# Optimization experiments

Hardware: AMD Instinct MI355X
Metric: run time of the kernel (lower is better)

The kernel has to match this reference:

```python
import jax, jax.numpy as jnp
import numpy as np

B, IMG, P, CIN = 4, 384, 16, 3
G = IMG // P            # 24 patches per side
NP = G * G              # 576 patch tokens
N = NP + 1              # +cls
D, H, L, MLP, NC = 768, 12, 12, 3072, 1000
HD = D // H
SCALE = HD ** -0.5
NUM_REL = (2 * G - 1) * (2 * G - 1) + 3   # (2*1-1)*(2G-1)*(2G-1)+3 = 2212
EPS = 1e-6


def gen_rel_index():
    # window (1, G, G): depth diff is always 0, reduces to 2D BEiT indexing
    coords = np.stack(np.meshgrid(np.arange(G), np.arange(G), indexing='ij')).reshape(2, -1)
    rel = (coords[:, :, None] - coords[:, None, :]).transpose(1, 2, 0).copy()  # (NP,NP,2)
    rel[:, :, 0] += G - 1
    rel[:, :, 1] += G - 1
    rel[:, :, 0] *= 2 * G - 1
    idx = np.zeros((N, N), dtype=np.int32)
    idx[1:, 1:] = rel.sum(-1)
    idx[0, :] = NUM_REL - 3
    idx[:, 0] = NUM_REL - 2
    idx[0, 0] = NUM_REL - 1
    return jnp.asarray(idx)


def setup_inputs() -> dict:
    key = jax.random.key(0)
    ks = jax.random.split(key, 20)
    s = 0.02
    inp = {
        'x': jax.random.normal(ks[0], (B, CIN, IMG, IMG), jnp.float32),
        'patch_w': s * jax.random.normal(ks[1], (D, CIN * P * P), jnp.float32),
        'patch_b': jnp.zeros((D,), jnp.float32),
        'cls_token': s * jax.random.normal(ks[2], (1, 1, D), jnp.float32),
        'pos_embed': s * jax.random.normal(ks[3], (1, N, D), jnp.float32),
        'ln1_w': jnp.ones((L, D), jnp.float32),
        'ln1_b': jnp.zeros((L, D), jnp.float32),
        'qkv_w': s * jax.random.normal(ks[4], (L, 3 * D, D), jnp.float32),
        'q_bias': jnp.zeros((L, D), jnp.float32),
        'v_bias': jnp.zeros((L, D), jnp.float32),
        'proj_w': s * jax.random.normal(ks[5], (L, D, D), jnp.float32),
        'proj_b': jnp.zeros((L, D), jnp.float32),
        'ln2_w': jnp.ones((L, D), jnp.float32),
        'ln2_b': jnp.zeros((L, D), jnp.float32),
        'fc1_w': s * jax.random.normal(ks[6], (L, MLP, D), jnp.float32),
        'fc1_b': jnp.zeros((L, MLP), jnp.float32),
        'fc2_w': s * jax.random.normal(ks[7], (L, D, MLP), jnp.float32),
        'fc2_b': jnp.zeros((L, D), jnp.float32),
        'rel_table': s * jax.random.normal(ks[8], (L, NUM_REL, H), jnp.float32),
        'fc_norm_w': jnp.ones((D,), jnp.float32),
        'fc_norm_b': jnp.zeros((D,), jnp.float32),
        'head_w': s * jax.random.normal(ks[9], (NC, D), jnp.float32),
        'head_b': jnp.zeros((NC,), jnp.float32),
        'rel_index': gen_rel_index(),
    }
    return inp


def _ln(x, w, b):
    m = x.mean(-1, keepdims=True)
    v = ((x - m) ** 2).mean(-1, keepdims=True)
    return (x - m) * jax.lax.rsqrt(v + EPS) * w + b


def _beit_fwd(x, patch_w, patch_b, cls_token, pos_embed,
              ln1_w, ln1_b, qkv_w, q_bias, v_bias, proj_w, proj_b,
              ln2_w, ln2_b, fc1_w, fc1_b, fc2_w, fc2_b, rel_table,
              fc_norm_w, fc_norm_b, head_w, head_b, rel_index):
    # patch embed: conv P x P stride P == reshape + matmul; patch vec order (c, ph, pw)
    patches = x.reshape(B, CIN, G, P, G, P).transpose(0, 2, 4, 1, 3, 5).reshape(B, NP, CIN * P * P)
    tok = patches @ patch_w.T + patch_b                      # (B, NP, D)
    h = jnp.concatenate([jnp.broadcast_to(cls_token, (B, 1, D)), tok], axis=1) + pos_embed

    def block(h, p):
        l1w, l1b, qw, qb, vb, pw, pb, l2w, l2b, f1w, f1b, f2w, f2b, rt = p
        y = _ln(h, l1w, l1b)
        bias = jnp.concatenate([qb, jnp.zeros_like(qb), vb])  # k_bias frozen zeros
        qkv = (y @ qw.T + bias).reshape(B, N, 3, H, HD).transpose(2, 0, 3, 1, 4)
        q, k, v = qkv[0] * SCALE, qkv[1], qkv[2]              # (B,H,N,HD)
        attn = jnp.einsum('bhnd,bhmd->bhnm', q, k)
        rel = rt[rel_index].transpose(2, 0, 1)                # (H,N,N)
        attn = jax.nn.softmax(attn + rel[None], axis=-1)
        o = jnp.einsum('bhnm,bhmd->bhnd', attn, v).transpose(0, 2, 1, 3).reshape(B, N, D)
        h = h + (o @ pw.T + pb)
        y = _ln(h, l2w, l2b)
        y = jax.nn.gelu(y @ f1w.T + f1b, approximate=False) @ f2w.T + f2b
        return h + y, None

    xs = (ln1_w, ln1_b, qkv_w, q_bias, v_bias, proj_w, proj_b,
          ln2_w, ln2_b, fc1_w, fc1_b, fc2_w, fc2_b, rel_table)
    h, _ = jax.lax.scan(block, h, xs)

    pooled = h[:, 1:].mean(axis=1)                            # global_pool='avg' drops cls
    return _ln(pooled, fc_norm_w, fc_norm_b) @ head_w.T + head_b  # (B, NC)


def reference(x, patch_w, patch_b, cls_token, pos_embed,
              ln1_w, ln1_b, qkv_w, q_bias, v_bias, proj_w, proj_b,
              ln2_w, ln2_b, fc1_w, fc1_b, fc2_w, fc2_b, rel_table,
              fc_norm_w, fc_norm_b, head_w, head_b, rel_index):
    return _beit_fwd(x, patch_w, patch_b, cls_token, pos_embed,
                     ln1_w, ln1_b, qkv_w, q_bias, v_bias, proj_w, proj_b,
                     ln2_w, ln2_b, fc1_w, fc1_b, fc2_w, fc2_b, rel_table,
                     fc_norm_w, fc_norm_b, head_w, head_b, rel_index)
```

## Files before the change

### kernel.cpp

```cpp
#include <hip/hip_runtime.h>
#include <math.h>

typedef unsigned short u16;
typedef __bf16 bf16x8_t __attribute__((ext_vector_type(8)));
typedef u16 u16x8 __attribute__((ext_vector_type(8)));
typedef float f32x4 __attribute__((ext_vector_type(4)));

#define CBATCH 4
#define CN 577
#define CNP 576
#define CD 768
#define CH 12
#define CHD 64
#define CL 12
#define CMLP 3072
#define CVP 640
#define CROWS (CBATCH*CN)
#define CROWSP 2432
#define CNN2 332929
#define CBH (CBATCH*CH)
#define CSKP 2
#define CSKF 4
#define CMT 37

__device__ __forceinline__ float b2f(u16 u){
  unsigned x = ((unsigned)u) << 16;
  return __builtin_bit_cast(float, x);
}
__device__ __forceinline__ u16 f2b(float f){
  unsigned x = __builtin_bit_cast(unsigned, f);
  unsigned r = x + 0x7fffu + ((x >> 16) & 1u);
  return (u16)(r >> 16);
}

__device__ __forceinline__ f32x4 MFMA(u16x8 a, u16x8 b, f32x4 c){
  return __builtin_amdgcn_mfma_f32_16x16x32_bf16(
      __builtin_bit_cast(bf16x8_t, a), __builtin_bit_cast(bf16x8_t, b), c, 0, 0, 0);
}

__device__ __forceinline__ void gl_lds16(const u16* g, u16* l){
  __builtin_amdgcn_global_load_lds(
      (const __attribute__((address_space(1))) unsigned int*)g,
      (__attribute__((address_space(3))) unsigned int*)l, 16, 0, 0);
}

__device__ __forceinline__ int xcd_chunk(int o, int nwg){
  int q8 = nwg >> 3, r8 = nwg & 7;
  int xcd = o & 7, sl = o >> 3;
  return (xcd < r8 ? xcd*(q8+1) : r8*(q8+1) + (xcd - r8)*q8) + sl;
}


__global__ void cvt_kernel(const float* __restrict__ src, u16* __restrict__ dst, int n){
  int i = (blockIdx.x * 256 + threadIdx.x) * 4;
  if(i < n){
    float4 v = *reinterpret_cast<const float4*>(src + i);
    ushort4 o;
    o.x = f2b(v.x); o.y = f2b(v.y); o.z = f2b(v.z); o.w = f2b(v.w);
    *reinterpret_cast<ushort4*>(dst + i) = o;
  }
}

__global__ void zero_kernel(u16* __restrict__ p, int n){
  int i = (blockIdx.x * 256 + threadIdx.x) * 8;
  if(i < n){
    u16x8 z = {0,0,0,0,0,0,0,0};
    *reinterpret_cast<u16x8*>(p + i) = z;
  }
}

__global__ void im2col_kernel(const float* __restrict__ x, u16* __restrict__ out){
  int id = blockIdx.x * 256 + threadIdx.x;
  if(id >= 2304*768) return;
  int col = id % 768, row = id / 768;
  int b = row / 576, p = row % 576;
  int gy = p / 24, gx = p % 24;
  int c = col >> 8, rem = col & 255, py = rem >> 4, px = rem & 15;
  float v = x[(((long)(b*3 + c)*384) + gy*16 + py)*384 + gx*16 + px];
  out[id] = f2b(v);
}

__global__ void clspos_kernel(const float* __restrict__ cls, const float* __restrict__ pos,
                              float* __restrict__ h){
  int id = blockIdx.x * 256 + threadIdx.x;
  if(id < CBATCH*CD){
    int b = id / CD, d = id % CD;
    h[(long)b*CN*CD + d] = cls[d] + pos[d];
  }
}

template<bool BF16OUT>
__global__ void ln_kernel(const float* __restrict__ x, const float* __restrict__ w,
                          const float* __restrict__ bsh, u16* __restrict__ yb,
                          float* __restrict__ yf){
  int r = blockIdx.x;
  int tid = threadIdx.x;
  const float* px = x + (long)r*CD;
  float v0 = px[tid], v1 = px[tid+256], v2 = px[tid+512];
  __shared__ float red[4];
  float s = v0 + v1 + v2;
  #pragma unroll
  for(int m=1;m<64;m<<=1) s += __shfl_xor(s, m);
  if((tid & 63) == 0) red[tid>>6] = s;
  __syncthreads();
  s = red[0]+red[1]+red[2]+red[3];
  float mean = s * (1.0f/768.0f);
  float d0 = v0-mean, d1 = v1-mean, d2 = v2-mean;
  float s2 = d0*d0 + d1*d1 + d2*d2;
  __syncthreads();
  #pragma unroll
  for(int m=1;m<64;m<<=1) s2 += __shfl_xor(s2, m);
  if((tid & 63) == 0) red[tid>>6] = s2;
  __syncthreads();
  s2 = red[0]+red[1]+red[2]+red[3];
  float rs = rsqrtf(s2*(1.0f/768.0f) + 1e-6f);
  float o0 = d0*rs*w[tid]     + bsh[tid];
  float o1 = d1*rs*w[tid+256] + bsh[tid+256];
  float o2 = d2*rs*w[tid+512] + bsh[tid+512];
  if(BF16OUT){
    yb[(long)r*CD + tid]     = f2b(o0);
    yb[(long)r*CD + tid+256] = f2b(o1);
    yb[(long)r*CD + tid+512] = f2b(o2);
  } else {
    yf[(long)r*CD + tid]     = o0;
    yf[(long)r*CD + tid+256] = o1;
    yf[(long)r*CD + tid+512] = o2;
  }
}

template<bool DOLN, int NSK>
__global__ void resid_ln_kernel(float* __restrict__ h, const float* __restrict__ part,
    const float* __restrict__ bias, const float* __restrict__ w,
    const float* __restrict__ bsh, u16* __restrict__ y){
  int r = blockIdx.x, tid = threadIdx.x;
  float v[3];
  #pragma unroll
  for(int j=0;j<3;j++){
    int c = tid + j*256;
    float t = h[(long)r*CD + c] + bias[c];
    #pragma unroll
    for(int sk=0; sk<NSK; sk++) t += part[((long)sk*CROWS + r)*CD + c];
    v[j] = t;
    h[(long)r*CD + c] = t;
  }
  if constexpr(DOLN){
    __shared__ float red[4];
    float s = v[0]+v[1]+v[2];
    #pragma unroll
    for(int m=1;m<64;m<<=1) s += __shfl_xor(s, m);
    if((tid & 63) == 0) red[tid>>6] = s;
    __syncthreads();
    s = red[0]+red[1]+red[2]+red[3];
    float mean = s * (1.0f/768.0f);
    float d0=v[0]-mean, d1=v[1]-mean, d2=v[2]-mean;
    float s2 = d0*d0+d1*d1+d2*d2;
    __syncthreads();
    #pragma unroll
    for(int m=1;m<64;m<<=1) s2 += __shfl_xor(s2, m);
    if((tid & 63) == 0) red[tid>>6] = s2;
    __syncthreads();
    s2 = red[0]+red[1]+red[2]+red[3];
    float rs = rsqrtf(s2*(1.0f/768.0f) + 1e-6f);
    y[(long)r*CD + tid]     = f2b(d0*rs*w[tid]     + bsh[tid]);
    y[(long)r*CD + tid+256] = f2b(d1*rs*w[tid+256] + bsh[tid+256]);
    y[(long)r*CD + tid+512] = f2b(d2*rs*w[tid+512] + bsh[tid+512]);
  }
}

__global__ void relbias_all_kernel(const int* __restrict__ ridx, const float* __restrict__ rtab,
                                   u16* __restrict__ attb){
  int id = blockIdx.x * 256 + threadIdx.x;
  if(id >= CNN2) return;
  int l = blockIdx.y;
  int idx = ridx[id];
  const float* rowp = rtab + (long)l*2212*12 + (long)idx*12;
  u16* dst = attb + (long)l*12*CNN2;
  #pragma unroll
  for(int hh=0; hh<12; hh++)
    dst[(long)hh*CNN2 + id] = f2b(rowp[hh]);
}

__global__ __launch_bounds__(256) void attn_kernel(
    const u16* __restrict__ q, const u16* __restrict__ k,
    const u16* __restrict__ vt, const u16* __restrict__ attb,
    u16* __restrict__ o_){
  __shared__ __align__(16) u16 lK[2][64*64];
  __shared__ __align__(16) u16 lV[2][64*64];
  __shared__ u16 pt[4][16*72];
  const int tid = threadIdx.x, lane = tid & 63, wv = tid >> 6;
  const int i15 = lane & 15, g4 = lane >> 4;
  const int o = blockIdx.y * 10 + blockIdx.x;
  const int cm = xcd_chunk(o, 480);
  const int bh = cm / 10, qt = cm % 10;
  const int b = bh / CH, hh = bh % CH;
  const int qrow0 = qt*64 + wv*16;
  const u16* qp = q + ((long)bh*CN + qrow0 + i15)*CHD + g4*8;
  u16x8 qa0 = *reinterpret_cast<const u16x8*>(qp);
  u16x8 qa1 = *reinterpret_cast<const u16x8*>(qp + 32);
  const u16* kbase = k + (long)bh*CN*CHD;
  const u16* vbase = vt + (long)bh*CHD*CVP;
  const u16* bb = attb + (long)hh*CNN2;

  const int srow = wv*16 + (lane>>3);
  const int scol = (lane&7)*8;
  const int sdst = wv*16*64;

  f32x4 po[4];
  float m[4], l[4];
  #pragma unroll
  for(int i=0;i<4;i++){ po[i]=(f32x4){0,0,0,0}; m[i]=-3.0e38f; l[i]=0.0f; }

  auto STAGE = [&](int t, int buf){
    const int kv0 = t*64;
    const u16* ks = kbase + ((long)(kv0 + srow))*CHD + scol;
    const u16* vs = vbase + ((long)srow)*CVP + kv0 + scol;
    gl_lds16(ks,          &lK[buf][sdst]);
    gl_lds16(ks + 8*CHD,  &lK[buf][sdst + 8*64]);
    gl_lds16(vs,          &lV[buf][sdst]);
    gl_lds16(vs + 8*CVP,  &lV[buf][sdst + 8*64]);
  };

  STAGE(0, 0);
  for(int t=0;t<10;t++){
    if(t+1 < 10){
      STAGE(t+1, (t+1)&1);
      asm volatile("s_waitcnt vmcnt(4)" ::: "memory");
    } else {
      asm volatile("s_waitcnt vmcnt(0)" ::: "memory");
    }
    __syncthreads();
    const int buf = t&1;
    const int kv0 = t*64;
    f32x4 sa[4];
    #pragma unroll
    for(int fc=0;fc<4;fc++){
      u16x8 k0 = *reinterpret_cast<const u16x8*>(&lK[buf][(fc*16+i15)*64 + g4*8]);
      u16x8 k1 = *reinterpret_cast<const u16x8*>(&lK[buf][(fc*16+i15)*64 + 32 + g4*8]);
      f32x4 z = (f32x4){0,0,0,0};
      z = MFMA(qa0, k0, z);
      z = MFMA(qa1, k1, z);
      sa[fc] = z;
    }
    float s[4][4];
    #pragma unroll
    for(int fc=0;fc<4;fc++){
      int kvc = kv0 + fc*16 + i15;
      bool valid = kvc < CN;
      #pragma unroll
      for(int r=0;r<4;r++){
        int qr = qrow0 + g4*4 + r;
        float bias = b2f(bb[(long)qr*CN + kvc]);
        s[fc][r] = valid ? (sa[fc][r] + bias) : -1e30f;
      }
    }
    float tm[4], ts[4], sc[4];
    #pragma unroll
    for(int r=0;r<4;r++)
      tm[r] = fmaxf(fmaxf(s[0][r],s[1][r]), fmaxf(s[2][r],s[3][r]));
    #pragma unroll
    for(int msk=1; msk<16; msk<<=1)
      #pragma unroll
      for(int r=0;r<4;r++)
        tm[r] = fmaxf(tm[r], __shfl_xor(tm[r], msk));
    #pragma unroll
    for(int r=0;r<4;r++){
      float mn = fmaxf(m[r], tm[r]);
      sc[r] = exp2f((m[r]-mn)*1.4426950408889634f);
      m[r] = mn;
      ts[r] = 0.f;
    }
    #pragma unroll
    for(int fc=0;fc<4;fc++)
      #pragma unroll
      for(int r=0;r<4;r++){
        float p = exp2f((s[fc][r]-m[r])*1.4426950408889634f);
        s[fc][r] = p; ts[r] += p;
      }
    #pragma unroll
    for(int msk=1; msk<16; msk<<=1)
      #pragma unroll
      for(int r=0;r<4;r++)
        ts[r] += __shfl_xor(ts[r], msk);
    #pragma unroll
    for(int r=0;r<4;r++) l[r] = l[r]*sc[r] + ts[r];
    #pragma unroll
    for(int d=0; d<4; d++)
      #pragma unroll
      for(int r=0;r<4;r++) po[d][r] *= sc[r];
    #pragma unroll
    for(int fc=0;fc<4;fc++)
      #pragma unroll
      for(int r=0;r<4;r++)
        pt[wv][(g4*4+r)*72 + fc*16 + i15] = f2b(s[fc][r]);
    u16x8 pa0 = *reinterpret_cast<const u16x8*>(&pt[wv][i15*72 + g4*8]);
    u16x8 pa1 = *reinterpret_cast<const u16x8*>(&pt[wv][i15*72 + 32 + g4*8]);
    #pragma unroll
    for(int d=0; d<4; d++){
      u16x8 v0 = *reinterpret_cast<const u16x8*>(&lV[buf][(d*16+i15)*64 + g4*8]);
      u16x8 v1 = *reinterpret_cast<const u16x8*>(&lV[buf][(d*16+i15)*64 + 32 + g4*8]);
      po[d] = MFMA(pa0, v0, po[d]);
      po[d] = MFMA(pa1, v1, po[d]);
    }
    __syncthreads();
  }
  #pragma unroll
  for(int d=0; d<4; d++)
    #pragma unroll
    for(int r=0;r<4;r++){
      int qr = qrow0 + g4*4 + r;
      if(qr < CN)
        o_[((long)(b*CN + qr))*CD + hh*CHD + d*16 + i15] = f2b(po[d][r] / l[r]);
    }
}

__global__ void pool_kernel(const float* __restrict__ h, float* __restrict__ pooled){
  int id = blockIdx.x * 256 + threadIdx.x;
  if(id >= CBATCH*CD) return;
  int b = id / CD, d = id % CD;
  const float* p = h + ((long)b*CN + 1)*CD + d;
  float s = 0.0f;
  for(int i=0;i<CNP;i++) s += p[(long)i*CD];
  pooled[id] = s * (1.0f/576.0f);
}

__global__ void head_kernel(const float* __restrict__ xn, const float* __restrict__ hw,
                            const float* __restrict__ hb, float* __restrict__ out){
  int nc = blockIdx.x;
  int tid = threadIdx.x;
  const float* wr = hw + (long)nc*CD;
  float w0 = wr[tid], w1 = wr[tid+256], w2 = wr[tid+512];
  __shared__ float red[4];
  for(int b=0;b<CBATCH;b++){
    const float* xr = xn + (long)b*CD;
    float s = w0*xr[tid] + w1*xr[tid+256] + w2*xr[tid+512];
    #pragma unroll
    for(int m=1;m<64;m<<=1) s += __shfl_xor(s, m);
    if((tid&63)==0) red[tid>>6] = s;
    __syncthreads();
    if(tid==0) out[b*1000 + nc] = red[0]+red[1]+red[2]+red[3] + hb[nc];
    __syncthreads();
  }
}


struct EpiArgs {
  float* hres;
  u16* outb;
  const float* bias;
  const float* pos;
  const float* qb;
  const float* vb;
  u16* q;
  u16* k;
  u16* vt;
  float* part;
};

enum { EPI_PATCH=0, EPI_QKV, EPI_GELU, EPI_PART };

template<int EPI>
__global__ __launch_bounds__(256,4) void gemm4(const u16* __restrict__ A, const u16* __restrict__ Bm,
    int M, int N, int K, int lda, int ldb, EpiArgs e){
  __shared__ __align__(16) u16 lA[3][64*32];
  __shared__ __align__(16) u16 lB[3][128*32];
  const int tid  = threadIdx.x;
  const int lane = tid & 63;
  const int wv   = tid >> 6;

  const int gx = gridDim.x, gy = gridDim.y;
  const int o = blockIdx.y * gx + blockIdx.x;
  const int cm = xcd_chunk(o, gx*gy);
  const int bn = (cm / gy) * 128;
  const int bm = (cm % gy) * 64;

  const int z  = blockIdx.z;
  A  += (long)z * K;
  Bm += (long)z * K;

  const int srow = wv*16 + (lane>>2);
  const u16* Asb = A  + (long)(bm + srow)*lda + (lane&3)*8;
  const u16* Bsb = Bm + (long)(bn + srow)*ldb + (lane&3)*8;
  const int ldst = wv*16*32;

  const int rbase = (wv>>1)*32;
  const int cbase = (wv&1)*64;
  const int i15 = lane & 15;
  const int k8off = (lane>>4)<<3;

  f32x4 acc[2][4];
  #pragma unroll
  for(int i=0;i<2;i++)
    #pragma unroll
    for(int j=0;j<4;j++)
      acc[i][j] = (f32x4){0.0f,0.0f,0.0f,0.0f};

  const int nkt = K >> 5;

  auto STAGE = [&](int kt, int slot){
    const u16* Ak = Asb + (long)kt*32;
    const u16* Bk = Bsb + (long)kt*32;
    gl_lds16(Ak,          &lA[slot][ldst]);
    gl_lds16(Bk,          &lB[slot][ldst]);
    gl_lds16(Bk + 64*ldb, &lB[slot][ldst + 64*32]);
  };

  STAGE(0, 0);
  if(nkt > 1) STAGE(1, 1);

  for(int kt=0; kt<nkt; kt++){
    if(kt+1 < nkt) asm volatile("s_waitcnt vmcnt(3) lgkmcnt(0)" ::: "memory");
    else           asm volatile("s_waitcnt vmcnt(0) lgkmcnt(0)" ::: "memory");
    __builtin_amdgcn_s_barrier();
    int nxt2 = kt + 2;
    if(nxt2 < nkt){ int sl = nxt2 % 3; STAGE(nxt2, sl); }
    const int cur = kt % 3;
    u16x8 af[2], bfr[4];
    #pragma unroll
    for(int f=0; f<2; f++)
      af[f]  = *reinterpret_cast<const u16x8*>(&lA[cur][(rbase + f*16 + i15)*32 + k8off]);
    #pragma unroll
    for(int f=0; f<4; f++)
      bfr[f] = *reinterpret_cast<const u16x8*>(&lB[cur][(cbase + f*16 + i15)*32 + k8off]);
    #pragma unroll
    for(int fr=0; fr<2; fr++)
      #pragma unroll
      for(int fc=0; fc<4; fc++)
        acc[fr][fc] = MFMA(af[fr], bfr[fc], acc[fr][fc]);
  }

  #pragma unroll
  for(int fr=0; fr<2; fr++){
    #pragma unroll
    for(int fc=0; fc<4; fc++){
      #pragma unroll
      for(int r=0;r<4;r++){
        int row = bm + rbase + fr*16 + ((lane>>4)<<2) + r;
        int col = bn + cbase + fc*16 + i15;
        if(row >= M || col >= N) continue;
        float v = acc[fr][fc][r];
        if constexpr(EPI == EPI_PATCH){
          int b = row/576, p = row%576;
          e.hres[((long)b*CN + 1 + p)*CD + col] = v + e.bias[col] + e.pos[(long)(1+p)*CD + col];
        } else if constexpr(EPI == EPI_QKV){
          int b = row/CN, n = row%CN;
          if(col < 768){
            int hh = col>>6, d = col&63;
            e.q[(((long)(b*CH+hh))*CN + n)*CHD + d] = f2b((v + e.qb[col]) * 0.125f);
          } else if(col < 1536){
            int c2 = col-768; int hh = c2>>6, d = c2&63;
            e.k[(((long)(b*CH+hh))*CN + n)*CHD + d] = f2b(v);
          } else {
            int c2 = col-1536; int hh = c2>>6, d = c2&63;
            e.vt[(((long)(b*CH+hh))*CHD + d)*CVP + n] = f2b(v + e.vb[c2]);
          }
        } else if constexpr(EPI == EPI_GELU){
          float t = v + e.bias[col];
          e.outb[(long)row*N + col] = f2b(t * 0.5f * (1.0f + erff(t*0.70710678118f)));
        } else {
          e.part[((long)z*CROWS + row)*CD + col] = v;
        }
      }
    }
  }
}


extern "C" void kernel_launch(void* const* d_in, const int* in_sizes, int n_in,
                              void* d_out, int out_size, void* d_ws, size_t ws_size,
                              hipStream_t stream){
  const float* x        = (const float*)d_in[0];
  const float* patch_w  = (const float*)d_in[1];
  const float* patch_b  = (const float*)d_in[2];
  const float* cls_tok  = (const float*)d_in[3];
  const float* pos_emb  = (const float*)d_in[4];
  const float* ln1_w    = (const float*)d_in[5];
  const float* ln1_b    = (const float*)d_in[6];
  const float* qkv_w    = (const float*)d_in[7];
  const float* q_bias   = (const float*)d_in[8];
  const float* v_bias   = (const float*)d_in[9];
  const float* proj_w   = (const float*)d_in[10];
  const float* proj_b   = (const float*)d_in[11];
  const float* ln2_w    = (const float*)d_in[12];
  const float* ln2_b    = (const float*)d_in[13];
  const float* fc1_w    = (const float*)d_in[14];
  const float* fc1_b    = (const float*)d_in[15];
  const float* fc2_w    = (const float*)d_in[16];
  const float* fc2_b    = (const float*)d_in[17];
  const float* rel_tab  = (const float*)d_in[18];
  const float* fcn_w    = (const float*)d_in[19];
  const float* fcn_b    = (const float*)d_in[20];
  const float* head_w   = (const float*)d_in[21];
  const float* head_b   = (const float*)d_in[22];
  const int*   rel_idx  = (const int*)d_in[23];
  float* out = (float*)d_out;
  char* ws = (char*)d_ws;

  size_t off = 0;
  auto alloc = [&](size_t bytes)->size_t{
    size_t o = off; off += (bytes + 255) & ~(size_t)255; return o;
  };
  const size_t OFF_H    = alloc((size_t)CROWS*CD*4);
  const size_t OFF_Y    = alloc((size_t)CROWSP*CD*2);
  const size_t OFF_Q    = alloc(((size_t)CBH*CN + 128)*CHD*2);
  const size_t OFF_K    = alloc(((size_t)CBH*CN + 128)*CHD*2);
  const size_t OFF_VT   = alloc((size_t)CBH*CHD*CVP*2);
  const size_t OFF_O    = alloc((size_t)CROWSP*CD*2);
  const size_t OFF_HID  = alloc((size_t)CROWSP*CMLP*2);
  const size_t OFF_PART = alloc((size_t)CSKF*CROWS*CD*4);
  const size_t OFF_ATTB = alloc(((size_t)CL*CH*CNN2 + 64*1024)*2);
  const size_t OFF_WP0  = alloc((size_t)768*768*2);
  const size_t OFF_WQA  = alloc((size_t)CL*2304*768*2);
  const size_t OFF_WPA  = alloc((size_t)CL*768*768*2);
  const size_t OFF_W1A  = alloc((size_t)CL*3072*768*2);
  const size_t OFF_W2A  = alloc((size_t)CL*768*3072*2);
  const size_t OFF_PL   = alloc((size_t)CBATCH*CD*4);
  const size_t OFF_NM   = alloc((size_t)CBATCH*CD*4);
  (void)ws_size; (void)in_sizes; (void)n_in; (void)out_size;

  float* h      = (float*)(ws + OFF_H);
  u16*   y      = (u16*)(ws + OFF_Y);
  u16*   qb_    = (u16*)(ws + OFF_Q);
  u16*   kb_    = (u16*)(ws + OFF_K);
  u16*   vt_    = (u16*)(ws + OFF_VT);
  u16*   o_     = (u16*)(ws + OFF_O);
  u16*   hid    = (u16*)(ws + OFF_HID);
  float* part   = (float*)(ws + OFF_PART);
  u16*   attb   = (u16*)(ws + OFF_ATTB);
  u16*   wp0    = (u16*)(ws + OFF_WP0);
  u16*   wqA    = (u16*)(ws + OFF_WQA);
  u16*   wpA    = (u16*)(ws + OFF_WPA);
  u16*   w1A    = (u16*)(ws + OFF_W1A);
  u16*   w2A    = (u16*)(ws + OFF_W2A);
  float* pooled = (float*)(ws + OFF_PL);
  float* normed = (float*)(ws + OFF_NM);

  auto cvt = [&](const float* src, u16* dst, long n){
    cvt_kernel<<<dim3((unsigned)((n/4 + 255)/256)), dim3(256), 0, stream>>>(src, dst, (int)n);
  };

  {
    int n = CBH*CHD*CVP;
    zero_kernel<<<dim3((n/8 + 255)/256), dim3(256), 0, stream>>>(vt_, n);
  }
  im2col_kernel<<<dim3((2304*768 + 255)/256), dim3(256), 0, stream>>>(x, hid);
  cvt(patch_w, wp0, 768*768);
  cvt(qkv_w,  wqA, (long)CL*2304*768);
  cvt(proj_w, wpA, (long)CL*768*768);
  cvt(fc1_w,  w1A, (long)CL*3072*768);
  cvt(fc2_w,  w2A, (long)CL*768*3072);
  relbias_all_kernel<<<dim3((CNN2 + 255)/256, CL), dim3(256), 0, stream>>>(
      rel_idx, rel_tab, attb);

  {
    EpiArgs e{}; e.hres = h; e.bias = patch_b; e.pos = pos_emb;
    gemm4<EPI_PATCH><<<dim3(6,36,1), dim3(256), 0, stream>>>(
        hid, wp0, 2304, 768, 768, 768, 768, e);
  }
  clspos_kernel<<<dim3(12), dim3(256), 0, stream>>>(cls_tok, pos_emb, h);

  ln_kernel<true><<<dim3(CROWS), dim3(256), 0, stream>>>(
      h, ln1_w, ln1_b, y, nullptr);

  for(int l=0; l<CL; l++){
    {
      EpiArgs e{}; e.qb = q_bias + l*CD; e.vb = v_bias + l*CD;
      e.q = qb_; e.k = kb_; e.vt = vt_;
      gemm4<EPI_QKV><<<dim3(18,CMT,1), dim3(256), 0, stream>>>(
          y, wqA + (long)l*2304*768, CROWS, 2304, 768, 768, 768, e);
    }
    attn_kernel<<<dim3(10, CBH), dim3(256), 0, stream>>>(
        qb_, kb_, vt_, attb + (long)l*CH*CNN2, o_);
    {
      EpiArgs e{}; e.part = part;
      gemm4<EPI_PART><<<dim3(6,CMT,CSKP), dim3(256), 0, stream>>>(
          o_, wpA + (long)l*768*768, CROWS, 768, 768/CSKP, 768, 768, e);
    }
    resid_ln_kernel<true,CSKP><<<dim3(CROWS), dim3(256), 0, stream>>>(
        h, part, proj_b + l*CD, ln2_w + l*CD, ln2_b + l*CD, y);
    {
      EpiArgs e{}; e.outb = hid; e.bias = fc1_b + l*CMLP;
      gemm4<EPI_GELU><<<dim3(24,CMT,1), dim3(256), 0, stream>>>(
          y, w1A + (long)l*3072*768, CROWS, 3072, 768, 768, 768, e);
    }
    {
      EpiArgs e{}; e.part = part;
      gemm4<EPI_PART><<<dim3(6,CMT,CSKF), dim3(256), 0, stream>>>(
          hid, w2A + (long)l*768*3072, CROWS, 768, 3072/CSKF, 3072, 3072, e);
    }
    if(l+1 < CL){
      resid_ln_kernel<true,CSKF><<<dim3(CROWS), dim3(256), 0, stream>>>(
          h, part, fc2_b + l*CD, ln1_w + (l+1)*CD, ln1_b + (l+1)*CD, y);
    } else {
      resid_ln_kernel<false,CSKF><<<dim3(CROWS), dim3(256), 0, stream>>>(
          h, part, fc2_b + l*CD, nullptr, nullptr, nullptr);
    }
  }

  pool_kernel<<<dim3(12), dim3(256), 0, stream>>>(h, pooled);
  ln_kernel<false><<<dim3(CBATCH), dim3(256), 0, stream>>>(
      pooled, fcn_w, fcn_b, nullptr, normed);
  head_kernel<<<dim3(1000), dim3(256), 0, stream>>>(normed, head_w, head_b, out);
}
```

Measured before the change: 2.087 ms.

## Switch GEMM to 128x128 tiles with A fragments loaded directly from global

The GEMM now uses 128x128 output tiles, with each wave computing a 64x64 sub-tile through a 4x4 array of MFMA accumulators. The A operand is no longer staged in LDS: each lane reads its MFMA fragment straight from global memory. Only B goes through LDS, with a double buffer instead of a triple buffer, and grid dimensions are halved along M to match. This raises arithmetic intensity per block and cuts LDS traffic, but the A loads sit on the critical path each k-step, the pipeline is shallower, register pressure is higher, and the grid has fewer blocks. Rows are padded to CROWSP, so the larger M tiles stay in bounds.

```diff
diff --git a/kernel.cpp b/kernel.cpp
--- a/kernel.cpp
+++ b/kernel.cpp
@@ -21,7 +21,6 @@
 #define CBH (CBATCH*CH)
 #define CSKP 2
 #define CSKF 4
-#define CMT 37
 
 __device__ __forceinline__ float b2f(u16 u){
   unsigned x = ((unsigned)u) << 16;
@@ -359,10 +358,9 @@
 enum { EPI_PATCH=0, EPI_QKV, EPI_GELU, EPI_PART };
 
 template<int EPI>
-__global__ __launch_bounds__(256,4) void gemm4(const u16* __restrict__ A, const u16* __restrict__ Bm,
+__global__ __launch_bounds__(256,4) void gemm5(const u16* __restrict__ A, const u16* __restrict__ Bm,
     int M, int N, int K, int lda, int ldb, EpiArgs e){
-  __shared__ __align__(16) u16 lA[3][64*32];
-  __shared__ __align__(16) u16 lB[3][128*32];
+  __shared__ __align__(16) u16 lB[2][128*32];
   const int tid  = threadIdx.x;
   const int lane = tid & 63;
   const int wv   = tid >> 6;
@@ -371,25 +369,26 @@
   const int o = blockIdx.y * gx + blockIdx.x;
   const int cm = xcd_chunk(o, gx*gy);
   const int bn = (cm / gy) * 128;
-  const int bm = (cm % gy) * 64;
+  const int bm = (cm % gy) * 128;
 
   const int z  = blockIdx.z;
   A  += (long)z * K;
   Bm += (long)z * K;
 
   const int srow = wv*16 + (lane>>2);
-  const u16* Asb = A  + (long)(bm + srow)*lda + (lane&3)*8;
   const u16* Bsb = Bm + (long)(bn + srow)*ldb + (lane&3)*8;
   const int ldst = wv*16*32;
 
-  const int rbase = (wv>>1)*32;
+  const int i15 = lane & 15;
+  const int g4  = lane >> 4;
+  const int rbase = (wv>>1)*64;
   const int cbase = (wv&1)*64;
-  const int i15 = lane & 15;
-  const int k8off = (lane>>4)<<3;
-
-  f32x4 acc[2][4];
-  #pragma unroll
-  for(int i=0;i<2;i++)
+
+  const u16* Ap = A + (long)(bm + rbase + i15)*lda + g4*8;
+
+  f32x4 acc[4][4];
+  #pragma unroll
+  for(int i=0;i<4;i++)
     #pragma unroll
     for(int j=0;j<4;j++)
       acc[i][j] = (f32x4){0.0f,0.0f,0.0f,0.0f};
@@ -397,39 +396,35 @@
   const int nkt = K >> 5;
 
   auto STAGE = [&](int kt, int slot){
-    const u16* Ak = Asb + (long)kt*32;
     const u16* Bk = Bsb + (long)kt*32;
-    gl_lds16(Ak,          &lA[slot][ldst]);
     gl_lds16(Bk,          &lB[slot][ldst]);
     gl_lds16(Bk + 64*ldb, &lB[slot][ldst + 64*32]);
   };
 
   STAGE(0, 0);
-  if(nkt > 1) STAGE(1, 1);
 
   for(int kt=0; kt<nkt; kt++){
-    if(kt+1 < nkt) asm volatile("s_waitcnt vmcnt(3) lgkmcnt(0)" ::: "memory");
-    else           asm volatile("s_waitcnt vmcnt(0) lgkmcnt(0)" ::: "memory");
+    asm volatile("s_waitcnt vmcnt(0)" ::: "memory");
     __builtin_amdgcn_s_barrier();
-    int nxt2 = kt + 2;
-    if(nxt2 < nkt){ int sl = nxt2 % 3; STAGE(nxt2, sl); }
-    const int cur = kt % 3;
-    u16x8 af[2], bfr[4];
-    #pragma unroll
-    for(int f=0; f<2; f++)
-      af[f]  = *reinterpret_cast<const u16x8*>(&lA[cur][(rbase + f*16 + i15)*32 + k8off]);
+    if(kt+1 < nkt) STAGE(kt+1, (kt+1)&1);
+    const int cur = kt & 1;
+    u16x8 af[4], bfr[4];
+    const u16* Ak = Ap + kt*32;
     #pragma unroll
     for(int f=0; f<4; f++)
-      bfr[f] = *reinterpret_cast<const u16x8*>(&lB[cur][(cbase + f*16 + i15)*32 + k8off]);
-    #pragma unroll
-    for(int fr=0; fr<2; fr++)
+      af[f] = *reinterpret_cast<const u16x8*>(Ak + (long)f*16*lda);
+    #pragma unroll
+    for(int f=0; f<4; f++)
+      bfr[f] = *reinterpret_cast<const u16x8*>(&lB[cur][(cbase + f*16 + i15)*32 + (g4<<3)]);
+    #pragma unroll
+    for(int fr=0; fr<4; fr++)
       #pragma unroll
       for(int fc=0; fc<4; fc++)
         acc[fr][fc] = MFMA(af[fr], bfr[fc], acc[fr][fc]);
   }
 
   #pragma unroll
-  for(int fr=0; fr<2; fr++){
+  for(int fr=0; fr<4; fr++){
     #pragma unroll
     for(int fc=0; fc<4; fc++){
       #pragma unroll
@@ -553,7 +548,7 @@
 
   {
     EpiArgs e{}; e.hres = h; e.bias = patch_b; e.pos = pos_emb;
-    gemm4<EPI_PATCH><<<dim3(6,36,1), dim3(256), 0, stream>>>(
+    gemm5<EPI_PATCH><<<dim3(6,18,1), dim3(256), 0, stream>>>(
         hid, wp0, 2304, 768, 768, 768, 768, e);
   }
   clspos_kernel<<<dim3(12), dim3(256), 0, stream>>>(cls_tok, pos_emb, h);
@@ -565,26 +560,26 @@
     {
       EpiArgs e{}; e.qb = q_bias + l*CD; e.vb = v_bias + l*CD;
       e.q = qb_; e.k = kb_; e.vt = vt_;
-      gemm4<EPI_QKV><<<dim3(18,CMT,1), dim3(256), 0, stream>>>(
+      gemm5<EPI_QKV><<<dim3(18,19,1), dim3(256), 0, stream>>>(
           y, wqA + (long)l*2304*768, CROWS, 2304, 768, 768, 768, e);
     }
     attn_kernel<<<dim3(10, CBH), dim3(256), 0, stream>>>(
         qb_, kb_, vt_, attb + (long)l*CH*CNN2, o_);
     {
       EpiArgs e{}; e.part = part;
-      gemm4<EPI_PART><<<dim3(6,CMT,CSKP), dim3(256), 0, stream>>>(
+      gemm5<EPI_PART><<<dim3(6,19,CSKP), dim3(256), 0, stream>>>(
           o_, wpA + (long)l*768*768, CROWS, 768, 768/CSKP, 768, 768, e);
     }
     resid_ln_kernel<true,CSKP><<<dim3(CROWS), dim3(256), 0, stream>>>(
         h, part, proj_b + l*CD, ln2_w + l*CD, ln2_b + l*CD, y);
     {
       EpiArgs e{}; e.outb = hid; e.bias = fc1_b + l*CMLP;
-      gemm4<EPI_GELU><<<dim3(24,CMT,1), dim3(256), 0, stream>>>(
+      gemm5<EPI_GELU><<<dim3(24,19,1), dim3(256), 0, stream>>>(
           y, w1A + (long)l*3072*768, CROWS, 3072, 768, 768, 768, e);
     }
     {
       EpiArgs e{}; e.part = part;
-      gemm4<EPI_PART><<<dim3(6,CMT,CSKF), dim3(256), 0, stream>>>(
+      gemm5<EPI_PART><<<dim3(6,19,CSKF), dim3(256), 0, stream>>>(
           hid, w2A + (long)l*768*3072, CROWS, 768, 3072/CSKF, 3072, 3072, e);
     }
     if(l+1 < CL){
```

Measured after the change: 2.898 ms. 38.9% more time.

## Process two query fragments per wave in attention and halve fc2 split-K

Applied to the files above, without the earlier changes.

Each attention wave now handles 32 query rows (two 16-row MFMA fragments) instead of 16, so every K/V tile staged in LDS and every register-loaded K/V fragment is reused twice. The grid shrinks from 480 to 240 blocks. The fc2 split-K factor also drops from 4 to 2, which cuts partial-sum traffic in the residual reduction but launches fewer fc2 blocks. The risks are higher register pressure and fewer blocks than compute units on the attention launch, which lowers occupancy and parallelism.

```diff
diff --git a/kernel.cpp b/kernel.cpp
--- a/kernel.cpp
+++ b/kernel.cpp
@@ -20,7 +20,7 @@
 #define CNN2 332929
 #define CBH (CBATCH*CH)
 #define CSKP 2
-#define CSKF 4
+#define CSKF 2
 #define CMT 37
 
 __device__ __forceinline__ float b2f(u16 u){
@@ -186,17 +186,21 @@
     u16* __restrict__ o_){
   __shared__ __align__(16) u16 lK[2][64*64];
   __shared__ __align__(16) u16 lV[2][64*64];
-  __shared__ u16 pt[4][16*72];
+  __shared__ u16 pt[4][32*72];
   const int tid = threadIdx.x, lane = tid & 63, wv = tid >> 6;
   const int i15 = lane & 15, g4 = lane >> 4;
-  const int o = blockIdx.y * 10 + blockIdx.x;
-  const int cm = xcd_chunk(o, 480);
-  const int bh = cm / 10, qt = cm % 10;
+  const int o = blockIdx.y * 5 + blockIdx.x;
+  const int cm = xcd_chunk(o, 240);
+  const int bh = cm / 5, qt = cm % 5;
   const int b = bh / CH, hh = bh % CH;
-  const int qrow0 = qt*64 + wv*16;
-  const u16* qp = q + ((long)bh*CN + qrow0 + i15)*CHD + g4*8;
-  u16x8 qa0 = *reinterpret_cast<const u16x8*>(qp);
-  u16x8 qa1 = *reinterpret_cast<const u16x8*>(qp + 32);
+  const int qrow0 = qt*128 + wv*32;
+  u16x8 qa[2][2];
+  #pragma unroll
+  for(int fr=0; fr<2; fr++){
+    const u16* qp = q + ((long)bh*CN + qrow0 + fr*16 + i15)*CHD + g4*8;
+    qa[fr][0] = *reinterpret_cast<const u16x8*>(qp);
+    qa[fr][1] = *reinterpret_cast<const u16x8*>(qp + 32);
+  }
   const u16* kbase = k + (long)bh*CN*CHD;
   const u16* vbase = vt + (long)bh*CHD*CVP;
   const u16* bb = attb + (long)hh*CNN2;
@@ -205,10 +209,12 @@
   const int scol = (lane&7)*8;
   const int sdst = wv*16*64;
 
-  f32x4 po[4];
-  float m[4], l[4];
-  #pragma unroll
-  for(int i=0;i<4;i++){ po[i]=(f32x4){0,0,0,0}; m[i]=-3.0e38f; l[i]=0.0f; }
+  f32x4 po[2][4];
+  float m[2][4], l[2][4];
+  #pragma unroll
+  for(int fr=0; fr<2; fr++)
+    #pragma unroll
+    for(int i=0;i<4;i++){ po[fr][i]=(f32x4){0,0,0,0}; m[fr][i]=-3.0e38f; l[fr][i]=0.0f; }
 
   auto STAGE = [&](int t, int buf){
     const int kv0 = t*64;
@@ -231,86 +237,101 @@
     __syncthreads();
     const int buf = t&1;
     const int kv0 = t*64;
-    f32x4 sa[4];
+    f32x4 sa[2][4];
     #pragma unroll
     for(int fc=0;fc<4;fc++){
       u16x8 k0 = *reinterpret_cast<const u16x8*>(&lK[buf][(fc*16+i15)*64 + g4*8]);
       u16x8 k1 = *reinterpret_cast<const u16x8*>(&lK[buf][(fc*16+i15)*64 + 32 + g4*8]);
-      f32x4 z = (f32x4){0,0,0,0};
-      z = MFMA(qa0, k0, z);
-      z = MFMA(qa1, k1, z);
-      sa[fc] = z;
-    }
-    float s[4][4];
-    #pragma unroll
-    for(int fc=0;fc<4;fc++){
-      int kvc = kv0 + fc*16 + i15;
-      bool valid = kvc < CN;
+      #pragma unroll
+      for(int fr=0;fr<2;fr++){
+        f32x4 z = (f32x4){0,0,0,0};
+        z = MFMA(qa[fr][0], k0, z);
+        z = MFMA(qa[fr][1], k1, z);
+        sa[fr][fc] = z;
+      }
+    }
+    float s[2][4][4];
+    #pragma unroll
+    for(int fr=0;fr<2;fr++){
+      #pragma unroll
+      for(int fc=0;fc<4;fc++){
+        int kvc = kv0 + fc*16 + i15;
+        bool valid = kvc < CN;
+        #pragma unroll
+        for(int r=0;r<4;r++){
+          int qr = qrow0 + fr*16 + g4*4 + r;
+          float bias = b2f(bb[(long)qr*CN + kvc]);
+          s[fr][fc][r] = valid ? (sa[fr][fc][r] + bias) : -1e30f;
+        }
+      }
+      float tm[4], ts[4], sc[4];
+      #pragma unroll
+      for(int r=0;r<4;r++)
+        tm[r] = fmaxf(fmaxf(s[fr][0][r],s[fr][1][r]), fmaxf(s[fr][2][r],s[fr][3][r]));
+      #pragma unroll
+      for(int msk=1; msk<16; msk<<=1)
+        #pragma unroll
+        for(int r=0;r<4;r++)
+          tm[r] = fmaxf(tm[r], __shfl_xor(tm[r], msk));
       #pragma unroll
       for(int r=0;r<4;r++){
-        int qr = qrow0 + g4*4 + r;
-        float bias = b2f(bb[(long)qr*CN + kvc]);
-        s[fc][r] = valid ? (sa[fc][r] + bias) : -1e30f;
+        float mn = fmaxf(m[fr][r], tm[r]);
+        sc[r] = exp2f((m[fr][r]-mn)*1.4426950408889634f);
+        m[fr][r] = mn;
+        ts[r] = 0.f;
       }
-    }
-    float tm[4], ts[4], sc[4];
-    #pragma unroll
-    for(int r=0;r<4;r++)
-      tm[r] = fmaxf(fmaxf(s[0][r],s[1][r]), fmaxf(s[2][r],s[3][r]));
-    #pragma unroll
-    for(int msk=1; msk<16; msk<<=1)
-      #pragma unroll
-      for(int r=0;r<4;r++)
-        tm[r] = fmaxf(tm[r], __shfl_xor(tm[r], msk));
-    #pragma unroll
-    for(int r=0;r<4;r++){
-      float mn = fmaxf(m[r], tm[r]);
-      sc[r] = exp2f((m[r]-mn)*1.4426950408889634f);
-      m[r] = mn;
-      ts[r] = 0.f;
-    }
-    #pragma unroll
-    for(int fc=0;fc<4;fc++)
-      #pragma unroll
-      for(int r=0;r<4;r++){
-        float p = exp2f((s[fc][r]-m[r])*1.4426950408889634f);
-        s[fc][r] = p; ts[r] += p;
-      }
-    #pragma unroll
-    for(int msk=1; msk<16; msk<<=1)
-      #pragma unroll
-      for(int r=0;r<4;r++)
-        ts[r] += __shfl_xor(ts[r], msk);
-    #pragma unroll
-    for(int r=0;r<4;r++) l[r] = l[r]*sc[r] + ts[r];
-    #pragma unroll
-    for(int d=0; d<4; d++)
-      #pragma unroll
-      for(int r=0;r<4;r++) po[d][r] *= sc[r];
-    #pragma unroll
-    for(int fc=0;fc<4;fc++)
-      #pragma unroll
-      for(int r=0;r<4;r++)
-        pt[wv][(g4*4+r)*72 + fc*16 + i15] = f2b(s[fc][r]);
-    u16x8 pa0 = *reinterpret_cast<const u16x8*>(&pt[wv][i15*72 + g4*8]);
-    u16x8 pa1 = *reinterpret_cast<const u16x8*>(&pt[wv][i15*72 + 32 + g4*8]);
+      #pragma unroll
+      for(int fc=0;fc<4;fc++)
+        #pragma unroll
+        for(int r=0;r<4;r++){
+          float p = exp2f((s[fr][fc][r]-m[fr][r])*1.4426950408889634f);
+          s[fr][fc][r] = p; ts[r] += p;
+        }
+      #pragma unroll
+      for(int msk=1; msk<16; msk<<=1)
+        #pragma unroll
+        for(int r=0;r<4;r++)
+          ts[r] += __shfl_xor(ts[r], msk);
+      #pragma unroll
+      for(int r=0;r<4;r++) l[fr][r] = l[fr][r]*sc[r] + ts[r];
+      #pragma unroll
+      for(int d=0; d<4; d++)
+        #pragma unroll
+        for(int r=0;r<4;r++) po[fr][d][r] *= sc[r];
+      #pragma unroll
+      for(int fc=0;fc<4;fc++)
+        #pragma unroll
+        for(int r=0;r<4;r++)
+          pt[wv][(fr*16 + g4*4+r)*72 + fc*16 + i15] = f2b(s[fr][fc][r]);
+    }
+    u16x8 pa[2][2];
+    #pragma unroll
+    for(int fr=0;fr<2;fr++){
+      pa[fr][0] = *reinterpret_cast<const u16x8*>(&pt[wv][(fr*16+i15)*72 + g4*8]);
+      pa[fr][1] = *reinterpret_cast<const u16x8*>(&pt[wv][(fr*16+i15)*72 + 32 + g4*8]);
+    }
     #pragma unroll
     for(int d=0; d<4; d++){
       u16x8 v0 = *reinterpret_cast<const u16x8*>(&lV[buf][(d*16+i15)*64 + g4*8]);
       u16x8 v1 = *reinterpret_cast<const u16x8*>(&lV[buf][(d*16+i15)*64 + 32 + g4*8]);
-      po[d] = MFMA(pa0, v0, po[d]);
-      po[d] = MFMA(pa1, v1, po[d]);
+      #pragma unroll
+      for(int fr=0;fr<2;fr++){
+        po[fr][d] = MFMA(pa[fr][0], v0, po[fr][d]);
+        po[fr][d] = MFMA(pa[fr][1], v1, po[fr][d]);
+      }
     }
     __syncthreads();
   }
   #pragma unroll
-  for(int d=0; d<4; d++)
-    #pragma unroll
-    for(int r=0;r<4;r++){
-      int qr = qrow0 + g4*4 + r;
-      if(qr < CN)
-        o_[((long)(b*CN + qr))*CD + hh*CHD + d*16 + i15] = f2b(po[d][r] / l[r]);
-    }
+  for(int fr=0;fr<2;fr++)
+    #pragma unroll
+    for(int d=0; d<4; d++)
+      #pragma unroll
+      for(int r=0;r<4;r++){
+        int qr = qrow0 + fr*16 + g4*4 + r;
+        if(qr < CN)
+          o_[((long)(b*CN + qr))*CD + hh*CHD + d*16 + i15] = f2b(po[fr][d][r] / l[fr][r]);
+      }
 }
 
 __global__ void pool_kernel(const float* __restrict__ h, float* __restrict__ pooled){
@@ -506,7 +527,7 @@
   const size_t OFF_VT   = alloc((size_t)CBH*CHD*CVP*2);
   const size_t OFF_O    = alloc((size_t)CROWSP*CD*2);
   const size_t OFF_HID  = alloc((size_t)CROWSP*CMLP*2);
-  const size_t OFF_PART = alloc((size_t)CSKF*CROWS*CD*4);
+  const size_t OFF_PART = alloc((size_t)4*CROWS*CD*4);
   const size_t OFF_ATTB = alloc(((size_t)CL*CH*CNN2 + 64*1024)*2);
   const size_t OFF_WP0  = alloc((size_t)768*768*2);
   const size_t OFF_WQA  = alloc((size_t)CL*2304*768*2);
@@ -568,7 +589,7 @@
       gemm4<EPI_QKV><<<dim3(18,CMT,1), dim3(256), 0, stream>>>(
           y, wqA + (long)l*2304*768, CROWS, 2304, 768, 768, 768, e);
     }
-    attn_kernel<<<dim3(10, CBH), dim3(256), 0, stream>>>(
+    attn_kernel<<<dim3(5, CBH), dim3(256), 0, stream>>>(
         qb_, kb_, vt_, attb + (long)l*CH*CNN2, o_);
     {
       EpiArgs e{}; e.part = part;
```

Result: slower. 3.131 ms (+50.0%).

## Pre-tile relative position bias and stage it through LDS in attention

Applied to the files above, without the earlier changes.

The relative-bias table is now precomputed into zero-padded 64x64 tiles that line up with the attention query/key tiles. The attention kernel loads each tile into LDS asynchronously alongside K and V, replacing the strided per-element global gathers. The fc2 split-K factor also drops from 4 to 2. The cost is extra LDS per block, more precomputed bias memory, and less split-K parallelism in fc2.

```diff
diff --git a/kernel.cpp b/kernel.cpp
--- a/kernel.cpp
+++ b/kernel.cpp
@@ -20,8 +20,10 @@
 #define CNN2 332929
 #define CBH (CBATCH*CH)
 #define CSKP 2
-#define CSKF 4
+#define CSKF 2
 #define CMT 37
+#define CQR 640
+#define CPLANE (CQR*64)
 
 __device__ __forceinline__ float b2f(u16 u){
   unsigned x = ((unsigned)u) << 16;
@@ -167,17 +169,27 @@
   }
 }
 
-__global__ void relbias_all_kernel(const int* __restrict__ ridx, const float* __restrict__ rtab,
-                                   u16* __restrict__ attb){
+__global__ void relbias_tiled_kernel(const int* __restrict__ ridx, const float* __restrict__ rtab,
+                                     u16* __restrict__ attbT){
   int id = blockIdx.x * 256 + threadIdx.x;
-  if(id >= CNN2) return;
-  int l = blockIdx.y;
-  int idx = ridx[id];
-  const float* rowp = rtab + (long)l*2212*12 + (long)idx*12;
-  u16* dst = attb + (long)l*12*CNN2;
-  #pragma unroll
-  for(int hh=0; hh<12; hh++)
-    dst[(long)hh*CNN2 + id] = f2b(rowp[hh]);
+  if(id >= 10*CQR*8) return;
+  int lh = blockIdx.y;
+  int l = lh / 12, hh = lh % 12;
+  int c8 = id & 7;
+  int qr = (id >> 3) % CQR;
+  int t  = (id >> 3) / CQR;
+  const float* rt = rtab + (long)l*2212*12;
+  u16 vals[8];
+  #pragma unroll
+  for(int j=0;j<8;j++){
+    int kvc = t*64 + c8*8 + j;
+    float v = 0.0f;
+    if(qr < CN && kvc < CN)
+      v = rt[(long)ridx[qr*CN + kvc]*12 + hh];
+    vals[j] = f2b(v);
+  }
+  *reinterpret_cast<u16x8*>(attbT + ((long)lh*10 + t)*CPLANE + (long)qr*64 + c8*8) =
+      *reinterpret_cast<const u16x8*>(vals);
 }
 
 __global__ __launch_bounds__(256) void attn_kernel(
@@ -186,6 +198,7 @@
     u16* __restrict__ o_){
   __shared__ __align__(16) u16 lK[2][64*64];
   __shared__ __align__(16) u16 lV[2][64*64];
+  __shared__ __align__(16) u16 lB[2][64*64];
   __shared__ u16 pt[4][16*72];
   const int tid = threadIdx.x, lane = tid & 63, wv = tid >> 6;
   const int i15 = lane & 15, g4 = lane >> 4;
@@ -199,7 +212,7 @@
   u16x8 qa1 = *reinterpret_cast<const u16x8*>(qp + 32);
   const u16* kbase = k + (long)bh*CN*CHD;
   const u16* vbase = vt + (long)bh*CHD*CVP;
-  const u16* bb = attb + (long)hh*CNN2;
+  const u16* abase = attb + (long)hh*10*CPLANE;
 
   const int srow = wv*16 + (lane>>3);
   const int scol = (lane&7)*8;
@@ -214,17 +227,20 @@
     const int kv0 = t*64;
     const u16* ks = kbase + ((long)(kv0 + srow))*CHD + scol;
     const u16* vs = vbase + ((long)srow)*CVP + kv0 + scol;
+    const u16* bs = abase + (long)t*CPLANE + (long)(qt*64 + srow)*64 + scol;
     gl_lds16(ks,          &lK[buf][sdst]);
     gl_lds16(ks + 8*CHD,  &lK[buf][sdst + 8*64]);
     gl_lds16(vs,          &lV[buf][sdst]);
     gl_lds16(vs + 8*CVP,  &lV[buf][sdst + 8*64]);
+    gl_lds16(bs,          &lB[buf][sdst]);
+    gl_lds16(bs + 8*64,   &lB[buf][sdst + 8*64]);
   };
 
   STAGE(0, 0);
   for(int t=0;t<10;t++){
     if(t+1 < 10){
       STAGE(t+1, (t+1)&1);
-      asm volatile("s_waitcnt vmcnt(4)" ::: "memory");
+      asm volatile("s_waitcnt vmcnt(6)" ::: "memory");
     } else {
       asm volatile("s_waitcnt vmcnt(0)" ::: "memory");
     }
@@ -248,8 +264,7 @@
       bool valid = kvc < CN;
       #pragma unroll
       for(int r=0;r<4;r++){
-        int qr = qrow0 + g4*4 + r;
-        float bias = b2f(bb[(long)qr*CN + kvc]);
+        float bias = b2f(lB[buf][(wv*16 + g4*4 + r)*64 + fc*16 + i15]);
         s[fc][r] = valid ? (sa[fc][r] + bias) : -1e30f;
       }
     }
@@ -506,8 +521,8 @@
   const size_t OFF_VT   = alloc((size_t)CBH*CHD*CVP*2);
   const size_t OFF_O    = alloc((size_t)CROWSP*CD*2);
   const size_t OFF_HID  = alloc((size_t)CROWSP*CMLP*2);
-  const size_t OFF_PART = alloc((size_t)CSKF*CROWS*CD*4);
-  const size_t OFF_ATTB = alloc(((size_t)CL*CH*CNN2 + 64*1024)*2);
+  const size_t OFF_PART = alloc((size_t)4*CROWS*CD*4);
+  const size_t OFF_ATTB = alloc((size_t)CL*CH*10*CPLANE*2);
   const size_t OFF_WP0  = alloc((size_t)768*768*2);
   const size_t OFF_WQA  = alloc((size_t)CL*2304*768*2);
   const size_t OFF_WPA  = alloc((size_t)CL*768*768*2);
@@ -548,7 +563,7 @@
   cvt(proj_w, wpA, (long)CL*768*768);
   cvt(fc1_w,  w1A, (long)CL*3072*768);
   cvt(fc2_w,  w2A, (long)CL*768*3072);
-  relbias_all_kernel<<<dim3((CNN2 + 255)/256, CL), dim3(256), 0, stream>>>(
+  relbias_tiled_kernel<<<dim3((10*CQR*8 + 255)/256, CL*CH), dim3(256), 0, stream>>>(
       rel_idx, rel_tab, attb);
 
   {
@@ -569,7 +584,7 @@
           y, wqA + (long)l*2304*768, CROWS, 2304, 768, 768, 768, e);
     }
     attn_kernel<<<dim3(10, CBH), dim3(256), 0, stream>>>(
-        qb_, kb_, vt_, attb + (long)l*CH*CNN2, o_);
+        qb_, kb_, vt_, attb + (long)l*CH*10*CPLANE, o_);
     {
       EpiArgs e{}; e.part = part;
       gemm4<EPI_PART><<<dim3(6,CMT,CSKP), dim3(256), 0, stream>>>(
```

New measurement: 2.280 ms. 1.09x slower.
